# Optimization experiments

Hardware: AMD Instinct MI355X
Metric: run time of the kernel (lower is better)

Reference implementation:

```python
import jax, jax.numpy as jnp
import numpy as np

NUM_NODES = 200000   # visited nodes in the temporal-KG subgraph
D = 64               # n_dims_in == n_dims_out
Q = 128              # number of query subgraphs (edges[:,0])
E = 1024             # edges per query group (equal-size groups)
NE = Q * E
RATIO = 0.0          # ratio_update
NEG_SLOPE = 0.01     # LeakyReLU default


def setup_inputs() -> dict:
    key = jax.random.key(0)
    ks = jax.random.split(key, 10)
    qid = jnp.repeat(jnp.arange(Q, dtype=jnp.int32), E)          # edges[:,0]
    src = jax.random.randint(ks[0], (NE,), 0, NUM_NODES, dtype=jnp.int32)
    dst = jax.random.randint(ks[1], (NE,), 0, NUM_NODES, dtype=jnp.int32)
    zeros = jnp.zeros((NE,), dtype=jnp.int32)
    # cols: 0=query idx, 1..5 unused metadata, 6=src (-2), 7=dst (-1)
    edges = jnp.stack([qid, zeros, zeros, zeros, zeros, zeros, src, dst], axis=1)
    std_g3 = np.sqrt(2.0 / (4 * D)).astype(np.float32)
    return {
        "node_score": jax.random.uniform(ks[2], (NUM_NODES,), dtype=jnp.float32),
        "node_repr": jax.random.normal(ks[3], (NUM_NODES, D), dtype=jnp.float32),
        "rel_emb": jax.random.normal(ks[4], (NE, D), dtype=jnp.float32),
        "query_src_ts_emb": jax.random.normal(ks[5], (Q, D), dtype=jnp.float32),
        "query_rel_emb": jax.random.normal(ks[6], (Q, D), dtype=jnp.float32),
        "Wq": jax.random.normal(ks[7], (4 * D, 4 * D), dtype=jnp.float32) * std_g3,
        "Wk": jax.random.normal(ks[8], (4 * D, 4 * D), dtype=jnp.float32) * std_g3,
        "W_lin": jax.random.normal(ks[9], (D, D), dtype=jnp.float32) * np.sqrt(2.0 / (2 * D)).astype(np.float32),
        "b_lin": jnp.zeros((D,), dtype=jnp.float32),
        "edges": edges,
        "max_edges": 128,
    }


def _segment_softmax(logits, seg, num_segments):
    # numerically stable softmax within segments (per src node)
    m = jax.ops.segment_max(logits, seg, num_segments=num_segments)
    ex = jnp.exp(logits - m[seg])
    s = jax.ops.segment_sum(ex, seg, num_segments=num_segments)
    return ex / s[seg]


def reference(node_score, node_repr, rel_emb, query_src_ts_emb, query_rel_emb,
              Wq, Wk, W_lin, b_lin, edges, max_edges):
    q = edges[:, 0]
    src = edges[:, 6]   # edges[:, -2]
    dst = edges[:, 7]   # edges[:, -1] (same as col 7 used for sparse rows)
    qs = query_src_ts_emb[q]   # [NE, D]
    qr = query_rel_emb[q]      # [NE, D]
    # G3 bilinear attention: sum(Q(left) * K(right), -1)
    left = jnp.concatenate([node_repr[src], rel_emb, qs, qr], axis=-1)   # [NE, 4D]
    right = jnp.concatenate([node_repr[dst], rel_emb, qs, qr], axis=-1)  # [NE, 4D]
    logits = jnp.sum((left @ Wq.T) * (right @ Wk.T), axis=-1)            # [NE]
    # segment softmax over src nodes, score propagation
    soft = _segment_softmax(logits, src, NUM_NODES)
    src_score = node_score[src]
    target_score = soft * src_score
    # top-k per query group (equal-size groups -> vectorized top_k)
    _, idx = jax.lax.top_k(target_score.reshape(Q, E), max_edges)        # [Q, k]
    flat = (jnp.arange(Q, dtype=idx.dtype)[:, None] * E + idx).reshape(-1)
    p_soft = soft[flat]
    p_src = src[flat]
    p_dst = dst[flat]
    p_src_score = src_score[flat]
    # sparse scatter: updated_node_score[dst] += softmax * src_score
    updated_node_score = jax.ops.segment_sum(p_soft * p_src_score, p_dst, num_segments=NUM_NODES)
    # representation update: rows src aggregate dst reprs weighted by softmax;
    # untouched nodes keep identity, touched src nodes keep ratio_update of self
    agg = jax.ops.segment_sum((1.0 - RATIO) * p_soft[:, None] * node_repr[p_dst],
                              p_src, num_segments=NUM_NODES)             # [N, D]
    is_src = jnp.zeros((NUM_NODES,), bool).at[p_src].set(True)
    diag = jnp.where(is_src, RATIO, 1.0)
    updated_repr = agg + diag[:, None] * node_repr
    # bypass_forward: LeakyReLU(Linear(.))
    out_repr = jax.nn.leaky_relu(updated_repr @ W_lin + b_lin, NEG_SLOPE)
    return updated_node_score, out_repr
```

## Files before the change

kernel.cpp:

```cpp
#include <hip/hip_runtime.h>

#define NNODES 200000
#define NQ     128
#define EPQ    1024
#define NE     (NQ*EPQ)
#define TOPK   128
#define NSEL   (NQ*TOPK)

__device__ __forceinline__ unsigned fkey(float f) {
  unsigned u = __float_as_uint(f);
  return (u & 0x80000000u) ? ~u : (u | 0x80000000u);
}
__device__ __forceinline__ float fdecode(unsigned k) {
  unsigned u = (k & 0x80000000u) ? (k ^ 0x80000000u) : ~k;
  return __uint_as_float(u);
}
__device__ __forceinline__ void fmarow(float* a, float x, const float4 n0, const float4 n1) {
  a[0] = fmaf(x, n0.x, a[0]); a[1] = fmaf(x, n0.y, a[1]);
  a[2] = fmaf(x, n0.z, a[2]); a[3] = fmaf(x, n0.w, a[3]);
  a[4] = fmaf(x, n1.x, a[4]); a[5] = fmaf(x, n1.y, a[5]);
  a[6] = fmaf(x, n1.z, a[6]); a[7] = fmaf(x, n1.w, a[7]);
}

typedef const __attribute__((address_space(1))) void* gas_ptr;
typedef __attribute__((address_space(3))) void* las_ptr;
__device__ __forceinline__ void gload16(const void* g, void* l) {
  __builtin_amdgcn_global_load_lds((gas_ptr)g, (las_ptr)l, 16, 0, 0);
}

__device__ __forceinline__ int nperm(int k) {
  const int q = k >> 2, p = k & 3;
  return (q & 1) * 64 + (q >> 1) * 4 + p;
}

__global__ __launch_bounds__(256) void k_init(unsigned* __restrict__ segmax,
                                              float* __restrict__ segsum,
                                              int* __restrict__ flag,
                                              float* __restrict__ outs) {
  const int i = blockIdx.x * 256 + threadIdx.x;
  if (i < NNODES) { segmax[i] = 0u; segsum[i] = 0.f; flag[i] = 0; outs[i] = 0.f; }
}

__global__ __launch_bounds__(256) void k_nmat(const float* __restrict__ Wq,
                                              const float* __restrict__ Wk,
                                              float* __restrict__ Nm) {
  __shared__ float ph[128];
  const int j = blockIdx.x;
  const int k = threadIdx.x & 127;
  const int ih = threadIdx.x >> 7;
  const int i0 = ih * 128;
  float a0 = 0.f, a1 = 0.f, a2 = 0.f, a3 = 0.f;
  for (int i = i0; i < i0 + 128; i += 4) {
    a0 = fmaf(Wq[(i + 0) * 256 + j], Wk[(i + 0) * 256 + k], a0);
    a1 = fmaf(Wq[(i + 1) * 256 + j], Wk[(i + 1) * 256 + k], a1);
    a2 = fmaf(Wq[(i + 2) * 256 + j], Wk[(i + 2) * 256 + k], a2);
    a3 = fmaf(Wq[(i + 3) * 256 + j], Wk[(i + 3) * 256 + k], a3);
  }
  const float p = (a0 + a1) + (a2 + a3);
  if (ih == 0) ph[k] = p;
  __syncthreads();
  if (ih == 1) Nm[j * 128 + nperm(k)] = ph[k] + p;
}

__global__ __launch_bounds__(256) void k_query(const float* __restrict__ Wq,
                                               const float* __restrict__ Wk,
                                               const float* __restrict__ qs_emb,
                                               const float* __restrict__ qr_emb,
                                               float* __restrict__ alpha,
                                               float* __restrict__ beta,
                                               float* __restrict__ cv) {
  __shared__ float sq[128];
  __shared__ float u[256], v[256];
  const int q = blockIdx.x, t = threadIdx.x;
  if (t < 64) sq[t] = qs_emb[q * 64 + t];
  else if (t < 128) sq[t] = qr_emb[q * 64 + (t - 64)];
  __syncthreads();
  {
    const float4* wq4 = (const float4*)(Wq + t * 256 + 128);
    const float4* wk4 = (const float4*)(Wk + t * 256 + 128);
    const float4* sq4 = (const float4*)sq;
    float uu = 0.f, vv = 0.f;
#pragma unroll 8
    for (int j = 0; j < 32; ++j) {
      const float4 a = wq4[j], b = wk4[j], s = sq4[j];
      uu = fmaf(a.x, s.x, fmaf(a.y, s.y, fmaf(a.z, s.z, fmaf(a.w, s.w, uu))));
      vv = fmaf(b.x, s.x, fmaf(b.y, s.y, fmaf(b.z, s.z, fmaf(b.w, s.w, vv))));
    }
    u[t] = uu; v[t] = vv;
  }
  __syncthreads();
  if (t < 128) {
    float a0 = 0.f, a1 = 0.f, a2 = 0.f, a3 = 0.f;
    for (int i = 0; i < 256; i += 4) {
      a0 = fmaf(Wq[(i + 0) * 256 + t], v[i + 0], a0);
      a1 = fmaf(Wq[(i + 1) * 256 + t], v[i + 1], a1);
      a2 = fmaf(Wq[(i + 2) * 256 + t], v[i + 2], a2);
      a3 = fmaf(Wq[(i + 3) * 256 + t], v[i + 3], a3);
    }
    alpha[q * 128 + t] = (a0 + a1) + (a2 + a3);
  } else {
    const int k = t - 128;
    float b0 = 0.f, b1 = 0.f, b2 = 0.f, b3 = 0.f;
    for (int i = 0; i < 256; i += 4) {
      b0 = fmaf(u[i + 0], Wk[(i + 0) * 256 + k], b0);
      b1 = fmaf(u[i + 1], Wk[(i + 1) * 256 + k], b1);
      b2 = fmaf(u[i + 2], Wk[(i + 2) * 256 + k], b2);
      b3 = fmaf(u[i + 3], Wk[(i + 3) * 256 + k], b3);
    }
    beta[q * 128 + k] = (b0 + b1) + (b2 + b3);
  }
  __syncthreads();
  if (t < 64) {
    float c = u[t] * v[t] + u[t + 64] * v[t + 64] + u[t + 128] * v[t + 128] + u[t + 192] * v[t + 192];
    c += __shfl_xor(c, 32, 64);
    c += __shfl_xor(c, 16, 64);
    c += __shfl_xor(c, 8, 64);
    c += __shfl_xor(c, 4, 64);
    c += __shfl_xor(c, 2, 64);
    c += __shfl_xor(c, 1, 64);
    if (t == 0) cv[q] = c;
  }
}

__global__ __launch_bounds__(512, 1) void k_logits(
    const float* __restrict__ repr, const float* __restrict__ rel,
    const int* __restrict__ edges, const float* __restrict__ Nm,
    const float* __restrict__ alpha, const float* __restrict__ beta,
    const float* __restrict__ cv, float* __restrict__ logits) {
  __shared__ float Nl[128 * 128];
  __shared__ float Xt[128][128];
  __shared__ float sA[128], sB[128];
  __shared__ int sSrc[128], sDst[128];
  const int t = threadIdx.x;
  const int e0 = blockIdx.x * 128;
  const int q = e0 >> 10;

  {
    const char* g = (const char*)Nm + (size_t)t * 16;
    char* l = (char*)Nl + (size_t)t * 16;
#pragma unroll
    for (int r = 0; r < 8; ++r) gload16(g + r * 8192, l + r * 8192);
  }

  if (t < 256) {
    const int el = t & 127;
    const int half = t >> 7;
    const int e = e0 + el;
    const float4* p;
    if (half == 0) {
      const int src = edges[e * 8 + 6];
      sSrc[el] = src;
      sDst[el] = edges[e * 8 + 7];
      p = (const float4*)(repr + (size_t)src * 64);
    } else {
      p = (const float4*)(rel + (size_t)e * 64);
    }
    const int jb = half * 64;
#pragma unroll
    for (int i = 0; i < 16; ++i) {
      const float4 v4 = p[i];
      const int j = jb + i * 4;
      Xt[j + 0][el] = v4.x; Xt[j + 1][el] = v4.y; Xt[j + 2][el] = v4.z; Xt[j + 3][el] = v4.w;
    }
  } else if (t < 384) {
    sA[t - 256] = alpha[q * 128 + (t - 256)];
  } else {
    sB[t - 384] = beta[q * 128 + (t - 384)];
  }
  __syncthreads();

  const int kg = t & 15, eg = t >> 4;
  const int k0 = kg * 8, eb = eg * 4;
  const int kf = kg * 4;
  float acc[4][8];
#pragma unroll
  for (int i = 0; i < 4; ++i)
#pragma unroll
    for (int m = 0; m < 8; ++m) acc[i][m] = 0.f;

#pragma unroll 4
  for (int j = 0; j < 128; ++j) {
    const float* __restrict__ Nrow = Nl + j * 128;
    const float4 n0 = *(const float4*)(Nrow + kf);
    const float4 n1 = *(const float4*)(Nrow + 64 + kf);
    const float4 xv = *(const float4*)(&Xt[j][eb]);
    fmarow(acc[0], xv.x, n0, n1);
    fmarow(acc[1], xv.y, n0, n1);
    fmarow(acc[2], xv.z, n0, n1);
    fmarow(acc[3], xv.w, n0, n1);
  }

  float aA[8], aB[8];
#pragma unroll
  for (int m = 0; m < 8; ++m) { aA[m] = sA[k0 + m]; aB[m] = sB[k0 + m]; }

  float part[4];
#pragma unroll
  for (int i = 0; i < 4; ++i) {
    const int el = eb + i;
    const int e = e0 + el;
    const float* xp;
    const float* yp;
    if (k0 < 64) {
      xp = repr + (size_t)sSrc[el] * 64 + k0;
      yp = repr + (size_t)sDst[el] * 64 + k0;
    } else {
      xp = rel + (size_t)e * 64 + (k0 - 64);
      yp = xp;
    }
    const float4 x0 = *(const float4*)xp;
    const float4 x1 = *(const float4*)(xp + 4);
    const float4 y0 = *(const float4*)yp;
    const float4 y1 = *(const float4*)(yp + 4);
    const float xs[8] = {x0.x, x0.y, x0.z, x0.w, x1.x, x1.y, x1.z, x1.w};
    const float ys[8] = {y0.x, y0.y, y0.z, y0.w, y1.x, y1.y, y1.z, y1.w};
    float p = 0.f;
#pragma unroll
    for (int m = 0; m < 8; ++m)
      p += (acc[i][m] + aB[m]) * ys[m] + aA[m] * xs[m];
    part[i] = p;
  }
#pragma unroll
  for (int i = 0; i < 4; ++i) {
    float p = part[i];
    p += __shfl_xor(p, 8, 64);
    p += __shfl_xor(p, 4, 64);
    p += __shfl_xor(p, 2, 64);
    p += __shfl_xor(p, 1, 64);
    part[i] = p;
  }
  if (kg == 0) {
    const float cq = cv[q];
#pragma unroll
    for (int i = 0; i < 4; ++i) logits[e0 + eb + i] = part[i] + cq;
  }
}

__global__ __launch_bounds__(256) void k_segmax(const float* __restrict__ logits,
                                                const int* __restrict__ edges,
                                                unsigned* __restrict__ segmax) {
  const int e = blockIdx.x * 256 + threadIdx.x;
  const int src = edges[e * 8 + 6];
  atomicMax(&segmax[src], fkey(logits[e]));
}

__global__ __launch_bounds__(256) void k_exsum(float* __restrict__ logits,
                                               const int* __restrict__ edges,
                                               const unsigned* __restrict__ segmax,
                                               float* __restrict__ segsum) {
  const int e = blockIdx.x * 256 + threadIdx.x;
  const int src = edges[e * 8 + 6];
  const float m = fdecode(segmax[src]);
  const float ex = expf(logits[e] - m);
  logits[e] = ex;
  atomicAdd(&segsum[src], ex);
}

__global__ __launch_bounds__(256) void k_topk(const float* __restrict__ ex,
                                              const float* __restrict__ segsum,
                                              const int* __restrict__ edges,
                                              const float* __restrict__ node_score,
                                              int* __restrict__ sel,
                                              int* __restrict__ flag,
                                              float* __restrict__ out_score,
                                              float* agg) {
  __shared__ unsigned keys[1024];
  __shared__ int hist[256];
  __shared__ int selEl[128];
  __shared__ int eqIdx[32];
  __shared__ int sB0, sRank, sCnt, sEq;
  const int q = blockIdx.x, t = threadIdx.x;
  for (int i = t; i < 1024; i += 256) {
    const int e = q * 1024 + i;
    const int src = edges[e * 8 + 6];
    const float ts = (ex[e] / segsum[src]) * node_score[src];
    keys[i] = fkey(ts);
  }
  unsigned prefix = 0, pmask = 0;
  int rank = 128;
  __syncthreads();
#pragma unroll
  for (int pass = 0; pass < 4; ++pass) {
    const int shift = 24 - 8 * pass;
    hist[t] = 0;
    __syncthreads();
    for (int i = t; i < 1024; i += 256) {
      const unsigned k = keys[i];
      if ((k & pmask) == prefix) atomicAdd(&hist[(k >> shift) & 255], 1);
    }
    __syncthreads();
    if (t < 64) {
      const int h0 = hist[4 * t], h1 = hist[4 * t + 1], h2 = hist[4 * t + 2], h3 = hist[4 * t + 3];
      const int s4 = h0 + h1 + h2 + h3;
      int S = s4;
      for (int d = 1; d < 64; d <<= 1) {
        const int o = __shfl_down(S, d, 64);
        if (t + d < 64) S += o;
      }
      const int Snext = S - s4;
      if (S >= rank && Snext < rank) {
        int r = rank - Snext;
        int b;
        if (r <= h3) b = 3;
        else if (r <= h3 + h2) { b = 2; r -= h3; }
        else if (r <= h3 + h2 + h1) { b = 1; r -= h3 + h2; }
        else { b = 0; r -= h3 + h2 + h1; }
        sB0 = 4 * t + b; sRank = r;
      }
    }
    __syncthreads();
    prefix |= ((unsigned)sB0) << shift;
    pmask |= 0xFFu << shift;
    rank = sRank;
    __syncthreads();
  }
  const unsigned thr = prefix;
  if (t == 0) { sCnt = 0; sEq = 0; }
  __syncthreads();
  for (int i = t; i < 1024; i += 256) {
    const unsigned k = keys[i];
    if (k > thr) { const int s = atomicAdd(&sCnt, 1); selEl[s] = i; }
    else if (k == thr) { const int j = atomicAdd(&sEq, 1); if (j < 32) eqIdx[j] = i; }
  }
  __syncthreads();
  if (t == 0) {
    int n = sEq; if (n > 32) n = 32;
    for (int a = 1; a < n; ++a) {
      const int v2 = eqIdx[a]; int b = a - 1;
      while (b >= 0 && eqIdx[b] > v2) { eqIdx[b + 1] = eqIdx[b]; --b; }
      eqIdx[b + 1] = v2;
    }
    for (int r2 = 0; r2 < rank; ++r2) selEl[sCnt + r2] = eqIdx[r2];
  }
  __syncthreads();
  if (t < 128) {
    const int el = selEl[t];
    const int e = q * 1024 + el;
    sel[q * 128 + t] = e;
    const int src = edges[e * 8 + 6];
    const int dst = edges[e * 8 + 7];
    const float soft = ex[e] / segsum[src];
    atomicAdd(&out_score[dst], soft * node_score[src]);
    flag[src] = 1;
  }
  __syncthreads();
  for (int i = t; i < 128 * 64; i += 256) {
    const int s = i >> 6, d = i & 63;
    const int e = q * 1024 + selEl[s];
    const int src = edges[e * 8 + 6];
    agg[(size_t)src * 64 + d] = 0.f;
  }
}

__global__ __launch_bounds__(256) void k_scatter(const int* __restrict__ sel,
                                                 const int* __restrict__ edges,
                                                 const float* __restrict__ ex,
                                                 const float* __restrict__ segsum,
                                                 const float* __restrict__ repr,
                                                 float* agg) {
  const int i = blockIdx.x * 4 + (threadIdx.x >> 6);
  const int d = threadIdx.x & 63;
  const int e = sel[i];
  const int src = edges[e * 8 + 6];
  const int dst = edges[e * 8 + 7];
  const float soft = ex[e] / segsum[src];
  atomicAdd(&agg[(size_t)src * 64 + d], soft * repr[(size_t)dst * 64 + d]);
}

#define FN 192
__global__ __launch_bounds__(192) void k_final(const float* __restrict__ repr,
                                               const float* agg,
                                               const int* __restrict__ flag,
                                               const float* __restrict__ Wl,
                                               const float* __restrict__ bl,
                                               float* outr) {
  __shared__ float Ut[64][FN];
  __shared__ float W[64][64];
  __shared__ float bs[64];
  const int t = threadIdx.x;
  const int n0blk = blockIdx.x * FN;
  for (int i = t; i < 4096; i += FN) W[i >> 6][i & 63] = Wl[i];
  if (t < 64) bs[t] = bl[t];
  {
    const int n = n0blk + t;
    const bool ok = n < NNODES;
    const float* rowp = repr;
    if (ok) rowp = (flag[n] ? agg : repr) + (size_t)n * 64;
#pragma unroll
    for (int i = 0; i < 16; ++i) {
      float4 v4 = ok ? ((const float4*)rowp)[i] : float4{0.f, 0.f, 0.f, 0.f};
      const int c = i * 4;
      Ut[c + 0][t] = v4.x; Ut[c + 1][t] = v4.y; Ut[c + 2][t] = v4.z; Ut[c + 3][t] = v4.w;
    }
  }
  __syncthreads();
  const int dg = t & 7, ng = t >> 3;
  const int d0 = dg * 8, nb = ng * 8;
  float acc[8][8];
#pragma unroll
  for (int i = 0; i < 8; ++i)
#pragma unroll
    for (int m = 0; m < 8; ++m) acc[i][m] = 0.f;
#pragma unroll 2
  for (int c = 0; c < 64; ++c) {
    const float4 w0 = *(const float4*)&W[c][d0];
    const float4 w1 = *(const float4*)&W[c][d0 + 4];
    const float4 u0 = *(const float4*)&Ut[c][nb];
    const float4 u1 = *(const float4*)&Ut[c][nb + 4];
    fmarow(acc[0], u0.x, w0, w1);
    fmarow(acc[1], u0.y, w0, w1);
    fmarow(acc[2], u0.z, w0, w1);
    fmarow(acc[3], u0.w, w0, w1);
    fmarow(acc[4], u1.x, w0, w1);
    fmarow(acc[5], u1.y, w0, w1);
    fmarow(acc[6], u1.z, w0, w1);
    fmarow(acc[7], u1.w, w0, w1);
  }
  float bb[8];
#pragma unroll
  for (int m = 0; m < 8; ++m) bb[m] = bs[d0 + m];
#pragma unroll
  for (int i = 0; i < 8; ++i) {
    const int n = n0blk + nb + i;
    if (n < NNODES) {
      float o[8];
#pragma unroll
      for (int m = 0; m < 8; ++m) {
        float v = acc[i][m] + bb[m];
        o[m] = v > 0.f ? v : 0.01f * v;
      }
      float4 o0 = {o[0], o[1], o[2], o[3]};
      float4 o1 = {o[4], o[5], o[6], o[7]};
      *(float4*)(outr + (size_t)n * 64 + d0) = o0;
      *(float4*)(outr + (size_t)n * 64 + d0 + 4) = o1;
    }
  }
}

extern "C" void kernel_launch(void* const* d_in, const int* in_sizes, int n_in,
                              void* d_out, int out_size, void* d_ws, size_t ws_size,
                              hipStream_t stream) {
  const float* node_score = (const float*)d_in[0];
  const float* node_repr  = (const float*)d_in[1];
  const float* rel_emb    = (const float*)d_in[2];
  const float* qs_emb     = (const float*)d_in[3];
  const float* qr_emb     = (const float*)d_in[4];
  const float* Wq         = (const float*)d_in[5];
  const float* Wk         = (const float*)d_in[6];
  const float* Wl         = (const float*)d_in[7];
  const float* bl         = (const float*)d_in[8];
  const int*   edges      = (const int*)d_in[9];

  float* out_score = (float*)d_out;
  float* out_repr  = out_score + NNODES;

  float* ws = (float*)d_ws;
  size_t o = 0;
  float* Nm      = ws + o; o += 128 * 128;
  float* alpha   = ws + o; o += NQ * 128;
  float* beta    = ws + o; o += NQ * 128;
  float* cv      = ws + o; o += NQ;
  float* exl     = ws + o; o += NE;
  unsigned* segmax = (unsigned*)(ws + o); o += NNODES;
  float* segsum  = ws + o; o += NNODES;
  int* sel       = (int*)(ws + o); o += NSEL;
  int* flag      = (int*)(ws + o); o += NNODES;

  k_init<<<(NNODES + 255) / 256, 256, 0, stream>>>(segmax, segsum, flag, out_score);
  k_nmat<<<128, 256, 0, stream>>>(Wq, Wk, Nm);
  k_query<<<NQ, 256, 0, stream>>>(Wq, Wk, qs_emb, qr_emb, alpha, beta, cv);
  k_logits<<<NE / 128, 512, 0, stream>>>(node_repr, rel_emb, edges, Nm, alpha, beta, cv, exl);
  k_segmax<<<NE / 256, 256, 0, stream>>>(exl, edges, segmax);
  k_exsum<<<NE / 256, 256, 0, stream>>>(exl, edges, segmax, segsum);
  k_topk<<<NQ, 256, 0, stream>>>(exl, segsum, edges, node_score, sel, flag, out_score, out_repr);
  k_scatter<<<NSEL / 4, 256, 0, stream>>>(sel, edges, exl, segsum, node_repr, out_repr);
  k_final<<<(NNODES + FN - 1) / FN, FN, 0, stream>>>(node_repr, out_repr, flag, Wl, bl, out_repr);
}
```

Measured before the change: 185.4 us.

## Double edges per logits block with row-major swizzled async staging

The logits kernel now handles 256 edges per block instead of 128, so each staged copy of the 128x128 N matrix in LDS is reused across twice as many edges. Each thread accumulates an 8x8 register tile instead of 4x8. Edge features are staged row-major with an XOR swizzle using direct global-to-LDS 16-byte loads. The src-repr half and the rel half are processed in two sequential phases sharing one buffer, replacing the transposed scalar LDS stores. This cuts N-matrix reloads and transpose store cost, but doubles the accumulator registers, halves the block count to 512, and adds an extra barrier between phases.

```diff
diff --git a/kernel.cpp b/kernel.cpp
--- a/kernel.cpp
+++ b/kernel.cpp
@@ -128,11 +128,11 @@
     const float* __restrict__ alpha, const float* __restrict__ beta,
     const float* __restrict__ cv, float* __restrict__ logits) {
   __shared__ float Nl[128 * 128];
-  __shared__ float Xt[128][128];
+  __shared__ float Xe[256 * 64];
   __shared__ float sA[128], sB[128];
-  __shared__ int sSrc[128], sDst[128];
+  __shared__ int sSrc[256], sDst[256];
   const int t = threadIdx.x;
-  const int e0 = blockIdx.x * 128;
+  const int e0 = blockIdx.x * 256;
   const int q = e0 >> 10;
 
   {
@@ -143,60 +143,101 @@
   }
 
   if (t < 256) {
-    const int el = t & 127;
-    const int half = t >> 7;
-    const int e = e0 + el;
-    const float4* p;
-    if (half == 0) {
-      const int src = edges[e * 8 + 6];
-      sSrc[el] = src;
-      sDst[el] = edges[e * 8 + 7];
-      p = (const float4*)(repr + (size_t)src * 64);
-    } else {
-      p = (const float4*)(rel + (size_t)e * 64);
-    }
-    const int jb = half * 64;
-#pragma unroll
-    for (int i = 0; i < 16; ++i) {
-      const float4 v4 = p[i];
-      const int j = jb + i * 4;
-      Xt[j + 0][el] = v4.x; Xt[j + 1][el] = v4.y; Xt[j + 2][el] = v4.z; Xt[j + 3][el] = v4.w;
-    }
+    sSrc[t] = edges[(size_t)(e0 + t) * 8 + 6];
+    sDst[t] = edges[(size_t)(e0 + t) * 8 + 7];
   } else if (t < 384) {
     sA[t - 256] = alpha[q * 128 + (t - 256)];
   } else {
     sB[t - 384] = beta[q * 128 + (t - 384)];
   }
+
+  const int elr = t >> 4, c = t & 15;
+  const int swzst = (elr >> 3) & 3;
+#pragma unroll
+  for (int r = 0; r < 8; ++r) {
+    const int el = r * 32 + elr;
+    const int src = edges[(size_t)(e0 + el) * 8 + 6];
+    const int cg = c ^ swzst;
+    gload16((const char*)repr + ((size_t)src * 64 + cg * 4) * 4,
+            (char*)Xe + ((size_t)el * 64 + c * 4) * 4);
+  }
   __syncthreads();
 
   const int kg = t & 15, eg = t >> 4;
-  const int k0 = kg * 8, eb = eg * 4;
+  const int k0 = kg * 8, eb = eg * 8;
   const int kf = kg * 4;
-  float acc[4][8];
-#pragma unroll
-  for (int i = 0; i < 4; ++i)
+  const int swz = eg & 3;
+  float acc[8][8];
+#pragma unroll
+  for (int i = 0; i < 8; ++i)
 #pragma unroll
     for (int m = 0; m < 8; ++m) acc[i][m] = 0.f;
 
-#pragma unroll 4
-  for (int j = 0; j < 128; ++j) {
-    const float* __restrict__ Nrow = Nl + j * 128;
-    const float4 n0 = *(const float4*)(Nrow + kf);
-    const float4 n1 = *(const float4*)(Nrow + 64 + kf);
-    const float4 xv = *(const float4*)(&Xt[j][eb]);
-    fmarow(acc[0], xv.x, n0, n1);
-    fmarow(acc[1], xv.y, n0, n1);
-    fmarow(acc[2], xv.z, n0, n1);
-    fmarow(acc[3], xv.w, n0, n1);
+#pragma unroll 2
+  for (int J = 0; J < 16; ++J) {
+    const float* __restrict__ Nr = Nl + (4 * J) * 128;
+    float4 n0[4], n1[4];
+#pragma unroll
+    for (int jj = 0; jj < 4; ++jj) {
+      n0[jj] = *(const float4*)(Nr + jj * 128 + kf);
+      n1[jj] = *(const float4*)(Nr + jj * 128 + 64 + kf);
+    }
+    const int ch = (J ^ swz) * 4;
+    float4 xv[8];
+#pragma unroll
+    for (int i = 0; i < 8; ++i)
+      xv[i] = *(const float4*)(Xe + (eb + i) * 64 + ch);
+#pragma unroll
+    for (int jj = 0; jj < 4; ++jj) {
+#pragma unroll
+      for (int i = 0; i < 8; ++i) {
+        const float xs = jj == 0 ? xv[i].x : jj == 1 ? xv[i].y : jj == 2 ? xv[i].z : xv[i].w;
+        fmarow(acc[i], xs, n0[jj], n1[jj]);
+      }
+    }
+  }
+  __syncthreads();
+
+#pragma unroll
+  for (int r = 0; r < 8; ++r) {
+    const int el = r * 32 + elr;
+    const int cg = c ^ swzst;
+    gload16((const char*)rel + ((size_t)(e0 + el) * 64 + cg * 4) * 4,
+            (char*)Xe + ((size_t)el * 64 + c * 4) * 4);
+  }
+  __syncthreads();
+
+#pragma unroll 2
+  for (int J = 0; J < 16; ++J) {
+    const float* __restrict__ Nr = Nl + (64 + 4 * J) * 128;
+    float4 n0[4], n1[4];
+#pragma unroll
+    for (int jj = 0; jj < 4; ++jj) {
+      n0[jj] = *(const float4*)(Nr + jj * 128 + kf);
+      n1[jj] = *(const float4*)(Nr + jj * 128 + 64 + kf);
+    }
+    const int ch = (J ^ swz) * 4;
+    float4 xv[8];
+#pragma unroll
+    for (int i = 0; i < 8; ++i)
+      xv[i] = *(const float4*)(Xe + (eb + i) * 64 + ch);
+#pragma unroll
+    for (int jj = 0; jj < 4; ++jj) {
+#pragma unroll
+      for (int i = 0; i < 8; ++i) {
+        const float xs = jj == 0 ? xv[i].x : jj == 1 ? xv[i].y : jj == 2 ? xv[i].z : xv[i].w;
+        fmarow(acc[i], xs, n0[jj], n1[jj]);
+      }
+    }
   }
 
   float aA[8], aB[8];
 #pragma unroll
   for (int m = 0; m < 8; ++m) { aA[m] = sA[k0 + m]; aB[m] = sB[k0 + m]; }
 
-  float part[4];
-#pragma unroll
-  for (int i = 0; i < 4; ++i) {
+  float part[8];
+#pragma unroll
+  for (int i = 0; i < 8; ++i) {
     const int el = eb + i;
     const int e = e0 + el;
     const float* xp;
@@ -221,7 +262,7 @@
     part[i] = p;
   }
 #pragma unroll
-  for (int i = 0; i < 4; ++i) {
+  for (int i = 0; i < 8; ++i) {
     float p = part[i];
     p += __shfl_xor(p, 8, 64);
     p += __shfl_xor(p, 4, 64);
@@ -231,8 +272,10 @@
   }
   if (kg == 0) {
     const float cq = cv[q];
-#pragma unroll
-    for (int i = 0; i < 4; ++i) logits[e0 + eb + i] = part[i] + cq;
+    float4 o0 = {part[0] + cq, part[1] + cq, part[2] + cq, part[3] + cq};
+    float4 o1 = {part[4] + cq, part[5] + cq, part[6] + cq, part[7] + cq};
+    *(float4*)(logits + e0 + eb) = o0;
+    *(float4*)(logits + e0 + eb + 4) = o1;
   }
 }
 
@@ -240,7 +283,7 @@
                                                 const int* __restrict__ edges,
                                                 unsigned* __restrict__ segmax) {
   const int e = blockIdx.x * 256 + threadIdx.x;
-  const int src = edges[e * 8 + 6];
+  const int src = edges[(size_t)e * 8 + 6];
   atomicMax(&segmax[src], fkey(logits[e]));
 }
 
@@ -249,7 +292,7 @@
                                                const unsigned* __restrict__ segmax,
                                                float* __restrict__ segsum) {
   const int e = blockIdx.x * 256 + threadIdx.x;
-  const int src = edges[e * 8 + 6];
+  const int src = edges[(size_t)e * 8 + 6];
   const float m = fdecode(segmax[src]);
   const float ex = expf(logits[e] - m);
   logits[e] = ex;
@@ -272,7 +315,7 @@
   const int q = blockIdx.x, t = threadIdx.x;
   for (int i = t; i < 1024; i += 256) {
     const int e = q * 1024 + i;
-    const int src = edges[e * 8 + 6];
+    const int src = edges[(size_t)e * 8 + 6];
     const float ts = (ex[e] / segsum[src]) * node_score[src];
     keys[i] = fkey(ts);
   }
@@ -337,8 +380,8 @@
     const int el = selEl[t];
     const int e = q * 1024 + el;
     sel[q * 128 + t] = e;
-    const int src = edges[e * 8 + 6];
-    const int dst = edges[e * 8 + 7];
+    const int src = edges[(size_t)e * 8 + 6];
+    const int dst = edges[(size_t)e * 8 + 7];
     const float soft = ex[e] / segsum[src];
     atomicAdd(&out_score[dst], soft * node_score[src]);
     flag[src] = 1;
@@ -347,7 +390,7 @@
   for (int i = t; i < 128 * 64; i += 256) {
     const int s = i >> 6, d = i & 63;
     const int e = q * 1024 + selEl[s];
-    const int src = edges[e * 8 + 6];
+    const int src = edges[(size_t)e * 8 + 6];
     agg[(size_t)src * 64 + d] = 0.f;
   }
 }
@@ -361,8 +404,8 @@
   const int i = blockIdx.x * 4 + (threadIdx.x >> 6);
   const int d = threadIdx.x & 63;
   const int e = sel[i];
-  const int src = edges[e * 8 + 6];
-  const int dst = edges[e * 8 + 7];
+  const int src = edges[(size_t)e * 8 + 6];
+  const int dst = edges[(size_t)e * 8 + 7];
   const float soft = ex[e] / segsum[src];
   atomicAdd(&agg[(size_t)src * 64 + d], soft * repr[(size_t)dst * 64 + d]);
 }
@@ -469,7 +512,7 @@
   k_init<<<(NNODES + 255) / 256, 256, 0, stream>>>(segmax, segsum, flag, out_score);
   k_nmat<<<128, 256, 0, stream>>>(Wq, Wk, Nm);
   k_query<<<NQ, 256, 0, stream>>>(Wq, Wk, qs_emb, qr_emb, alpha, beta, cv);
-  k_logits<<<NE / 128, 512, 0, stream>>>(node_repr, rel_emb, edges, Nm, alpha, beta, cv, exl);
+  k_logits<<<NE / 256, 512, 0, stream>>>(node_repr, rel_emb, edges, Nm, alpha, beta, cv, exl);
   k_segmax<<<NE / 256, 256, 0, stream>>>(exl, edges, segmax);
   k_exsum<<<NE / 256, 256, 0, stream>>>(exl, edges, segmax, segsum);
   k_topk<<<NQ, 256, 0, stream>>>(exl, segsum, edges, node_score, sel, flag, out_score, out_repr);
```

Measured after the change: 175.6 us. 5.3% less time.
